# Performance work log

Hardware: AMD Instinct MI355X
Metric: run time of the kernel (lower is better)

## Reference

```python
import jax, jax.numpy as jnp
import numpy as np

N, A, B, C = 256, 1024, 64, 16


def setup_inputs() -> dict:
    key = jax.random.key(0)
    k1, k2, k3 = jax.random.split(key, 3)
    x = jax.random.normal(k1, (N, A), dtype=jnp.float32)
    weight = jax.random.normal(k2, (A, B * C), dtype=jnp.float32) * 0.02
    bias = jax.random.normal(k3, (B,), dtype=jnp.float32) * 0.02
    return {"x": x, "weight": weight, "bias": bias}


def reference(x, weight, bias):
    # x: [N, A]; weight: [A, B*C]; bias: [B]
    n = x.shape[0]
    mat = (x @ weight).reshape(n, B, C)              # [N, B, C]
    # pairwise L1 over the C (kernel) axis -> [N, N, B]
    l1 = jnp.abs(mat[:, None, :, :] - mat[None, :, :, :]).sum(axis=-1)
    # exp(-L1), sum over the first (broadcast) axis as in the torch code,
    # which includes the self term exp(0)=1
    out = jnp.exp(-l1).sum(axis=0) + bias            # [N, B]
    return out
```

## Files before the change

kernel.cpp:

```cpp
#include <hip/hip_runtime.h>
#include <hip/hip_bf16.h>

#define LOG2E 1.4426950408889634f

typedef __bf16 bf16x8 __attribute__((ext_vector_type(8)));
typedef float  f32x4  __attribute__((ext_vector_type(4)));

__device__ inline unsigned pack2(float lo, float hi){
  __hip_bfloat162 h = __float22bfloat162_rn(make_float2(lo, hi));
  return *reinterpret_cast<unsigned*>(&h);
}

__global__ __launch_bounds__(1024) void k_gemm_ks(const float* __restrict__ X,
                                                  const float* __restrict__ Wm,
                                                  float* __restrict__ P){
  __shared__ unsigned short As[4][64 * 72];
  __shared__ unsigned short Bs[4][64 * 72];
  const int m0 = blockIdx.x * 64, n0 = blockIdx.y * 64;
  const int k0 = blockIdx.z * 256;
  const int t = threadIdx.x;
  const int lane = t & 63, w = t >> 6;
  const int g = t >> 8, s = t & 255;
  const int r16 = lane & 15, quad = lane >> 4;
  const int wrow = (w & 3) * 16, wcol = (w >> 2) * 16;

  const int ar = s >> 2, aq = s & 3;
  const int bc = s & 15, bg = s >> 4;
  const float* ap = X + (size_t)(m0 + ar) * 1024 + k0 + g * 64 + aq * 16;
  const float* bp = Wm + (size_t)(k0 + g * 64) * 1024 + n0 + bc * 4;

  float4 pa[4], pb[4];
  #pragma unroll
  for (int r = 0; r < 4; ++r) pa[r] = *(const float4*)(ap + r * 4);
  #pragma unroll
  for (int r = 0; r < 4; ++r) pb[r] = *(const float4*)(bp + (size_t)(4 * bg + r) * 1024);

  {
    unsigned short* d = &As[g][ar * 72 + aq * 16];
    uint4 o;
    o.x = pack2(pa[0].x, pa[0].y); o.y = pack2(pa[0].z, pa[0].w);
    o.z = pack2(pa[1].x, pa[1].y); o.w = pack2(pa[1].z, pa[1].w);
    *(uint4*)d = o;
    o.x = pack2(pa[2].x, pa[2].y); o.y = pack2(pa[2].z, pa[2].w);
    o.z = pack2(pa[3].x, pa[3].y); o.w = pack2(pa[3].z, pa[3].w);
    *(uint4*)(d + 8) = o;
  }
  {
    #pragma unroll
    for (int e = 0; e < 4; ++e){
      const int n = bc * 4 + e;
      uint2 o;
      o.x = pack2(((const float*)&pb[0])[e], ((const float*)&pb[1])[e]);
      o.y = pack2(((const float*)&pb[2])[e], ((const float*)&pb[3])[e]);
      const int cw = (bg >> 1) ^ ((n >> 3) & 7);
      *(uint2*)(&Bs[g][n * 72 + cw * 8 + (bg & 1) * 4]) = o;
    }
  }
  __syncthreads();

  f32x4 acc0, acc1;
  #pragma unroll
  for (int e = 0; e < 4; ++e){ acc0[e] = 0.f; acc1[e] = 0.f; }
  const int nn = wcol + r16;
  const int nsw = (nn >> 3) & 7;
  #pragma unroll
  for (int gg = 0; gg < 4; ++gg){
    bf16x8 a0 = *(const bf16x8*)(&As[gg][(wrow + r16) * 72 + quad * 8]);
    bf16x8 a1 = *(const bf16x8*)(&As[gg][(wrow + r16) * 72 + 32 + quad * 8]);
    bf16x8 b0 = *(const bf16x8*)(&Bs[gg][nn * 72 + (((quad    ) ^ nsw) * 8)]);
    bf16x8 b1 = *(const bf16x8*)(&Bs[gg][nn * 72 + (((quad + 4) ^ nsw) * 8)]);
    acc0 = __builtin_amdgcn_mfma_f32_16x16x32_bf16(a0, b0, acc0, 0, 0, 0);
    acc1 = __builtin_amdgcn_mfma_f32_16x16x32_bf16(a1, b1, acc1, 0, 0, 0);
  }
  float* Pz = P + (size_t)blockIdx.z * 64 * 4096 + (size_t)((n0 + wcol) >> 4) * 4096;
  #pragma unroll
  for (int r = 0; r < 4; ++r){
    const int row = m0 + wrow + quad * 4 + r;
    Pz[row * 16 + r16] = acc0[r] + acc1[r];
  }
}

__global__ __launch_bounds__(1024) void k_pair(const float* __restrict__ P,
                                               const float* __restrict__ bias,
                                               float* __restrict__ out){
  __shared__ float L[256 * 20];
  __shared__ float red[16][64];
  const int b = blockIdx.x >> 2, jc = blockIdx.x & 3;
  const int t = threadIdx.x, lane = t & 63, w = t >> 6;

  {
    const int i = t >> 2, q = t & 3;
    const float* base = P + (size_t)b * 4096 + t * 4;
    float4 s0 = *(const float4*)(base);
    float4 s1 = *(const float4*)(base + 262144);
    float4 s2 = *(const float4*)(base + 524288);
    float4 s3 = *(const float4*)(base + 786432);
    float4 r;
    r.x = (s0.x + s1.x) + (s2.x + s3.x);
    r.y = (s0.y + s1.y) + (s2.y + s3.y);
    r.z = (s0.z + s1.z) + (s2.z + s3.z);
    r.w = (s0.w + s1.w) + (s2.w + s3.w);
    *(float4*)(&L[i * 20 + q * 4]) = r;
  }
  __syncthreads();

  const int j = jc * 64 + lane;
  float oj[16];
  #pragma unroll
  for (int q = 0; q < 4; ++q){
    float4 v = *(const float4*)(&L[j * 20 + q * 4]);
    oj[q*4+0] = v.x; oj[q*4+1] = v.y; oj[q*4+2] = v.z; oj[q*4+3] = v.w;
  }

  float acc = 0.f;
  const int i0 = w * 16;
  #pragma unroll 4
  for (int ii = i0; ii < i0 + 16; ++ii){
    const float4* fr = (const float4*)(&L[ii * 20]);
    float4 f0 = fr[0], f1 = fr[1], f2 = fr[2], f3 = fr[3];
    float p0 = fabsf(oj[0]  - f0.x) + fabsf(oj[1]  - f0.y)
             + fabsf(oj[2]  - f0.z) + fabsf(oj[3]  - f0.w);
    float p1 = fabsf(oj[4]  - f1.x) + fabsf(oj[5]  - f1.y)
             + fabsf(oj[6]  - f1.z) + fabsf(oj[7]  - f1.w);
    float p2 = fabsf(oj[8]  - f2.x) + fabsf(oj[9]  - f2.y)
             + fabsf(oj[10] - f2.z) + fabsf(oj[11] - f2.w);
    float p3 = fabsf(oj[12] - f3.x) + fabsf(oj[13] - f3.y)
             + fabsf(oj[14] - f3.z) + fabsf(oj[15] - f3.w);
    acc += exp2f(-LOG2E * ((p0 + p1) + (p2 + p3)));
  }
  red[w][lane] = acc;
  __syncthreads();
  if (w == 0){
    float tot = 0.f;
    #pragma unroll
    for (int ww = 0; ww < 16; ++ww) tot += red[ww][lane];
    out[(size_t)j * 64 + b] = tot + bias[b];
  }
}

extern "C" void kernel_launch(void* const* d_in, const int* in_sizes, int n_in,
                              void* d_out, int out_size, void* d_ws, size_t ws_size,
                              hipStream_t stream){
  const float* x    = (const float*)d_in[0];
  const float* W    = (const float*)d_in[1];
  const float* bias = (const float*)d_in[2];
  float* out = (float*)d_out;
  float* P   = (float*)d_ws;

  k_gemm_ks<<<dim3(4, 16, 4), 1024, 0, stream>>>(x, W, P);
  k_pair<<<256, 1024, 0, stream>>>(P, bias, out);
}
```

Baseline: 74.08 us.

## Fuse GEMM and pairwise kernels into one launch with a grid barrier

Merges the split-K GEMM kernel and the pairwise L1/exp kernel into one persistent 256-block kernel. The two phases are separated by a software grid barrier built on an atomic counter. This removes one kernel launch and the gap between the two kernels. In exchange it relies on all 256 blocks being co-resident and adds atomic spin-wait overhead. The ticket-based target keeps the counter valid across repeated calls.

```diff
diff --git a/kernel.cpp b/kernel.cpp
--- a/kernel.cpp
+++ b/kernel.cpp
@@ -11,130 +11,154 @@
   return *reinterpret_cast<unsigned*>(&h);
 }
 
-__global__ __launch_bounds__(1024) void k_gemm_ks(const float* __restrict__ X,
-                                                  const float* __restrict__ Wm,
-                                                  float* __restrict__ P){
-  __shared__ unsigned short As[4][64 * 72];
-  __shared__ unsigned short Bs[4][64 * 72];
-  const int m0 = blockIdx.x * 64, n0 = blockIdx.y * 64;
-  const int k0 = blockIdx.z * 256;
+__device__ unsigned g_bar;
+
+__device__ inline void grid_barrier(){
+  __threadfence();
+  __syncthreads();
+  if (threadIdx.x == 0){
+    unsigned ticket = __hip_atomic_fetch_add(&g_bar, 1u, __ATOMIC_ACQ_REL,
+                                             __HIP_MEMORY_SCOPE_AGENT);
+    unsigned target = (ticket / 256u + 1u) * 256u;
+    while (__hip_atomic_load(&g_bar, __ATOMIC_ACQUIRE,
+                             __HIP_MEMORY_SCOPE_AGENT) < target)
+      __builtin_amdgcn_s_sleep(2);
+  }
+  __syncthreads();
+  __threadfence();
+}
+
+__global__ __launch_bounds__(1024) void k_fused(const float* __restrict__ X,
+                                                const float* __restrict__ Wm,
+                                                const float* __restrict__ bias,
+                                                float* __restrict__ out,
+                                                float* __restrict__ P){
+  __shared__ __align__(16) char smem[73728];
+  unsigned short* As = (unsigned short*)smem;
+  unsigned short* Bs = (unsigned short*)(smem + 36864);
+
+  const int bid = blockIdx.x;
   const int t = threadIdx.x;
   const int lane = t & 63, w = t >> 6;
-  const int g = t >> 8, s = t & 255;
   const int r16 = lane & 15, quad = lane >> 4;
-  const int wrow = (w & 3) * 16, wcol = (w >> 2) * 16;
-
-  const int ar = s >> 2, aq = s & 3;
-  const int bc = s & 15, bg = s >> 4;
-  const float* ap = X + (size_t)(m0 + ar) * 1024 + k0 + g * 64 + aq * 16;
-  const float* bp = Wm + (size_t)(k0 + g * 64) * 1024 + n0 + bc * 4;
-
-  float4 pa[4], pb[4];
-  #pragma unroll
-  for (int r = 0; r < 4; ++r) pa[r] = *(const float4*)(ap + r * 4);
-  #pragma unroll
-  for (int r = 0; r < 4; ++r) pb[r] = *(const float4*)(bp + (size_t)(4 * bg + r) * 1024);
 
   {
-    unsigned short* d = &As[g][ar * 72 + aq * 16];
-    uint4 o;
-    o.x = pack2(pa[0].x, pa[0].y); o.y = pack2(pa[0].z, pa[0].w);
-    o.z = pack2(pa[1].x, pa[1].y); o.w = pack2(pa[1].z, pa[1].w);
-    *(uint4*)d = o;
-    o.x = pack2(pa[2].x, pa[2].y); o.y = pack2(pa[2].z, pa[2].w);
-    o.z = pack2(pa[3].x, pa[3].y); o.w = pack2(pa[3].z, pa[3].w);
-    *(uint4*)(d + 8) = o;
-  }
-  {
+    const int m0 = (bid & 3) * 64, n0 = ((bid >> 2) & 15) * 64;
+    const int ks = bid >> 6, k0 = ks * 256;
+    const int g = t >> 8, s = t & 255;
+    const int wrow = (w & 3) * 16, wcol = (w >> 2) * 16;
+
+    const int ar = s >> 2, aq = s & 3;
+    const int bc = s & 15, bg = s >> 4;
+    const float* ap = X + (size_t)(m0 + ar) * 1024 + k0 + g * 64 + aq * 16;
+    const float* bp = Wm + (size_t)(k0 + g * 64) * 1024 + n0 + bc * 4;
+
+    float4 pa[4], pb[4];
     #pragma unroll
-    for (int e = 0; e < 4; ++e){
-      const int n = bc * 4 + e;
-      uint2 o;
-      o.x = pack2(((const float*)&pb[0])[e], ((const float*)&pb[1])[e]);
-      o.y = pack2(((const float*)&pb[2])[e], ((const float*)&pb[3])[e]);
-      const int cw = (bg >> 1) ^ ((n >> 3) & 7);
-      *(uint2*)(&Bs[g][n * 72 + cw * 8 + (bg & 1) * 4]) = o;
+    for (int r = 0; r < 4; ++r) pa[r] = *(const float4*)(ap + r * 4);
+    #pragma unroll
+    for (int r = 0; r < 4; ++r) pb[r] = *(const float4*)(bp + (size_t)(4 * bg + r) * 1024);
+
+    {
+      unsigned short* d = &As[g * 4608 + ar * 72 + aq * 16];
+      uint4 o;
+      o.x = pack2(pa[0].x, pa[0].y); o.y = pack2(pa[0].z, pa[0].w);
+      o.z = pack2(pa[1].x, pa[1].y); o.w = pack2(pa[1].z, pa[1].w);
+      *(uint4*)d = o;
+      o.x = pack2(pa[2].x, pa[2].y); o.y = pack2(pa[2].z, pa[2].w);
+      o.z = pack2(pa[3].x, pa[3].y); o.w = pack2(pa[3].z, pa[3].w);
+      *(uint4*)(d + 8) = o;
+    }
+    {
+      #pragma unroll
+      for (int e = 0; e < 4; ++e){
+        const int n = bc * 4 + e;
+        uint2 o;
+        o.x = pack2(((const float*)&pb[0])[e], ((const float*)&pb[1])[e]);
+        o.y = pack2(((const float*)&pb[2])[e], ((const float*)&pb[3])[e]);
+        const int cw = (bg >> 1) ^ ((n >> 3) & 7);
+        *(uint2*)(&Bs[g * 4608 + n * 72 + cw * 8 + (bg & 1) * 4]) = o;
+      }
+    }
+    __syncthreads();
+
+    f32x4 acc0, acc1;
+    #pragma unroll
+    for (int e = 0; e < 4; ++e){ acc0[e] = 0.f; acc1[e] = 0.f; }
+    const int nn = wcol + r16;
+    const int nsw = (nn >> 3) & 7;
+    #pragma unroll
+    for (int gg = 0; gg < 4; ++gg){
+      bf16x8 a0 = *(const bf16x8*)(&As[gg * 4608 + (wrow + r16) * 72 + quad * 8]);
+      bf16x8 a1 = *(const bf16x8*)(&As[gg * 4608 + (wrow + r16) * 72 + 32 + quad * 8]);
+      bf16x8 b0 = *(const bf16x8*)(&Bs[gg * 4608 + nn * 72 + (((quad    ) ^ nsw) * 8)]);
+      bf16x8 b1 = *(const bf16x8*)(&Bs[gg * 4608 + nn * 72 + (((quad + 4) ^ nsw) * 8)]);
+      acc0 = __builtin_amdgcn_mfma_f32_16x16x32_bf16(a0, b0, acc0, 0, 0, 0);
+      acc1 = __builtin_amdgcn_mfma_f32_16x16x32_bf16(a1, b1, acc1, 0, 0, 0);
+    }
+    float* Pz = P + (size_t)ks * 262144 + (size_t)((n0 + wcol) >> 4) * 4096;
+    #pragma unroll
+    for (int r = 0; r < 4; ++r){
+      const int row = m0 + wrow + quad * 4 + r;
+      Pz[row * 16 + r16] = acc0[r] + acc1[r];
     }
   }
-  __syncthreads();
 
-  f32x4 acc0, acc1;
-  #pragma unroll
-  for (int e = 0; e < 4; ++e){ acc0[e] = 0.f; acc1[e] = 0.f; }
-  const int nn = wcol + r16;
-  const int nsw = (nn >> 3) & 7;
-  #pragma unroll
-  for (int gg = 0; gg < 4; ++gg){
-    bf16x8 a0 = *(const bf16x8*)(&As[gg][(wrow + r16) * 72 + quad * 8]);
-    bf16x8 a1 = *(const bf16x8*)(&As[gg][(wrow + r16) * 72 + 32 + quad * 8]);
-    bf16x8 b0 = *(const bf16x8*)(&Bs[gg][nn * 72 + (((quad    ) ^ nsw) * 8)]);
-    bf16x8 b1 = *(const bf16x8*)(&Bs[gg][nn * 72 + (((quad + 4) ^ nsw) * 8)]);
-    acc0 = __builtin_amdgcn_mfma_f32_16x16x32_bf16(a0, b0, acc0, 0, 0, 0);
-    acc1 = __builtin_amdgcn_mfma_f32_16x16x32_bf16(a1, b1, acc1, 0, 0, 0);
-  }
-  float* Pz = P + (size_t)blockIdx.z * 64 * 4096 + (size_t)((n0 + wcol) >> 4) * 4096;
-  #pragma unroll
-  for (int r = 0; r < 4; ++r){
-    const int row = m0 + wrow + quad * 4 + r;
-    Pz[row * 16 + r16] = acc0[r] + acc1[r];
-  }
-}
-
-__global__ __launch_bounds__(1024) void k_pair(const float* __restrict__ P,
-                                               const float* __restrict__ bias,
-                                               float* __restrict__ out){
-  __shared__ float L[256 * 20];
-  __shared__ float red[16][64];
-  const int b = blockIdx.x >> 2, jc = blockIdx.x & 3;
-  const int t = threadIdx.x, lane = t & 63, w = t >> 6;
+  grid_barrier();
 
   {
-    const int i = t >> 2, q = t & 3;
-    const float* base = P + (size_t)b * 4096 + t * 4;
-    float4 s0 = *(const float4*)(base);
-    float4 s1 = *(const float4*)(base + 262144);
-    float4 s2 = *(const float4*)(base + 524288);
-    float4 s3 = *(const float4*)(base + 786432);
-    float4 r;
-    r.x = (s0.x + s1.x) + (s2.x + s3.x);
-    r.y = (s0.y + s1.y) + (s2.y + s3.y);
-    r.z = (s0.z + s1.z) + (s2.z + s3.z);
-    r.w = (s0.w + s1.w) + (s2.w + s3.w);
-    *(float4*)(&L[i * 20 + q * 4]) = r;
-  }
-  __syncthreads();
+    float* L   = (float*)smem;
+    float* red = (float*)(smem + 20480);
+    const int b = bid >> 2, jc = bid & 3;
 
-  const int j = jc * 64 + lane;
-  float oj[16];
-  #pragma unroll
-  for (int q = 0; q < 4; ++q){
-    float4 v = *(const float4*)(&L[j * 20 + q * 4]);
-    oj[q*4+0] = v.x; oj[q*4+1] = v.y; oj[q*4+2] = v.z; oj[q*4+3] = v.w;
-  }
+    {
+      const int i = t >> 2, q = t & 3;
+      const float* base = P + (size_t)b * 4096 + t * 4;
+      float4 s0 = *(const float4*)(base);
+      float4 s1 = *(const float4*)(base + 262144);
+      float4 s2 = *(const float4*)(base + 524288);
+      float4 s3 = *(const float4*)(base + 786432);
+      float4 r;
+      r.x = (s0.x + s1.x) + (s2.x + s3.x);
+      r.y = (s0.y + s1.y) + (s2.y + s3.y);
+      r.z = (s0.z + s1.z) + (s2.z + s3.z);
+      r.w = (s0.w + s1.w) + (s2.w + s3.w);
+      *(float4*)(&L[i * 20 + q * 4]) = r;
+    }
+    __syncthreads();
 
-  float acc = 0.f;
-  const int i0 = w * 16;
-  #pragma unroll 4
-  for (int ii = i0; ii < i0 + 16; ++ii){
-    const float4* fr = (const float4*)(&L[ii * 20]);
-    float4 f0 = fr[0], f1 = fr[1], f2 = fr[2], f3 = fr[3];
-    float p0 = fabsf(oj[0]  - f0.x) + fabsf(oj[1]  - f0.y)
-             + fabsf(oj[2]  - f0.z) + fabsf(oj[3]  - f0.w);
-    float p1 = fabsf(oj[4]  - f1.x) + fabsf(oj[5]  - f1.y)
-             + fabsf(oj[6]  - f1.z) + fabsf(oj[7]  - f1.w);
-    float p2 = fabsf(oj[8]  - f2.x) + fabsf(oj[9]  - f2.y)
-             + fabsf(oj[10] - f2.z) + fabsf(oj[11] - f2.w);
-    float p3 = fabsf(oj[12] - f3.x) + fabsf(oj[13] - f3.y)
-             + fabsf(oj[14] - f3.z) + fabsf(oj[15] - f3.w);
-    acc += exp2f(-LOG2E * ((p0 + p1) + (p2 + p3)));
-  }
-  red[w][lane] = acc;
-  __syncthreads();
-  if (w == 0){
-    float tot = 0.f;
+    const int j = jc * 64 + lane;
+    float oj[16];
     #pragma unroll
-    for (int ww = 0; ww < 16; ++ww) tot += red[ww][lane];
-    out[(size_t)j * 64 + b] = tot + bias[b];
+    for (int q = 0; q < 4; ++q){
+      float4 v = *(const float4*)(&L[j * 20 + q * 4]);
+      oj[q*4+0] = v.x; oj[q*4+1] = v.y; oj[q*4+2] = v.z; oj[q*4+3] = v.w;
+    }
+
+    float acc = 0.f;
+    const int i0 = w * 16;
+    #pragma unroll 4
+    for (int ii = i0; ii < i0 + 16; ++ii){
+      const float4* fr = (const float4*)(&L[ii * 20]);
+      float4 f0 = fr[0], f1 = fr[1], f2 = fr[2], f3 = fr[3];
+      float p0 = fabsf(oj[0]  - f0.x) + fabsf(oj[1]  - f0.y)
+               + fabsf(oj[2]  - f0.z) + fabsf(oj[3]  - f0.w);
+      float p1 = fabsf(oj[4]  - f1.x) + fabsf(oj[5]  - f1.y)
+               + fabsf(oj[6]  - f1.z) + fabsf(oj[7]  - f1.w);
+      float p2 = fabsf(oj[8]  - f2.x) + fabsf(oj[9]  - f2.y)
+               + fabsf(oj[10] - f2.z) + fabsf(oj[11] - f2.w);
+      float p3 = fabsf(oj[12] - f3.x) + fabsf(oj[13] - f3.y)
+               + fabsf(oj[14] - f3.z) + fabsf(oj[15] - f3.w);
+      acc += exp2f(-LOG2E * ((p0 + p1) + (p2 + p3)));
+    }
+    red[w * 64 + lane] = acc;
+    __syncthreads();
+    if (w == 0){
+      float tot = 0.f;
+      #pragma unroll
+      for (int ww = 0; ww < 16; ++ww) tot += red[ww * 64 + lane];
+      out[(size_t)j * 64 + b] = tot + bias[b];
+    }
   }
 }
 
@@ -147,6 +171,5 @@
   float* out = (float*)d_out;
   float* P   = (float*)d_ws;
 
-  k_gemm_ks<<<dim3(4, 16, 4), 1024, 0, stream>>>(x, W, P);
-  k_pair<<<256, 1024, 0, stream>>>(P, bias, out);
+  k_fused<<<256, 1024, 0, stream>>>(x, W, bias, out, P);
 }
```

Measured after the change: 259.4 us. +250.2%, slower.

## Replace split-K GEMM with full-K tiles reduced in shared memory

Applied to the files above, without the earlier changes.

The GEMM now uses 32x32 output tiles over the full K=1024. Each block holds all of K in shared memory (144KB) and four wave groups split K, reducing their partials through LDS. This removes the split-K partial buffer, so the pair kernel reads one slice instead of summing four. The cost is large LDS use, one block per CU, and more redundant global loads of X and W across tiles.

```diff
diff --git a/kernel.cpp b/kernel.cpp
--- a/kernel.cpp
+++ b/kernel.cpp
@@ -11,72 +11,96 @@
   return *reinterpret_cast<unsigned*>(&h);
 }
 
-__global__ __launch_bounds__(1024) void k_gemm_ks(const float* __restrict__ X,
-                                                  const float* __restrict__ Wm,
-                                                  float* __restrict__ P){
-  __shared__ unsigned short As[4][64 * 72];
-  __shared__ unsigned short Bs[4][64 * 72];
-  const int m0 = blockIdx.x * 64, n0 = blockIdx.y * 64;
-  const int k0 = blockIdx.z * 256;
-  const int t = threadIdx.x;
-  const int lane = t & 63, w = t >> 6;
-  const int g = t >> 8, s = t & 255;
+__global__ __launch_bounds__(1024) void k_gemm(const float* __restrict__ X,
+                                               const float* __restrict__ Wm,
+                                               float* __restrict__ P){
+  __shared__ __align__(16) char smem[147456];
+  unsigned short* As = (unsigned short*)smem;
+  unsigned short* Bs = (unsigned short*)(smem + 73728);
+  float* red = (float*)smem;
+
+  const int nt = blockIdx.x, mt = blockIdx.y;
+  const int m0 = mt * 32, n0 = nt * 32;
+  const int t = threadIdx.x, lane = t & 63, w = t >> 6;
   const int r16 = lane & 15, quad = lane >> 4;
-  const int wrow = (w & 3) * 16, wcol = (w >> 2) * 16;
-
-  const int ar = s >> 2, aq = s & 3;
-  const int bc = s & 15, bg = s >> 4;
-  const float* ap = X + (size_t)(m0 + ar) * 1024 + k0 + g * 64 + aq * 16;
-  const float* bp = Wm + (size_t)(k0 + g * 64) * 1024 + n0 + bc * 4;
-
-  float4 pa[4], pb[4];
-  #pragma unroll
-  for (int r = 0; r < 4; ++r) pa[r] = *(const float4*)(ap + r * 4);
-  #pragma unroll
-  for (int r = 0; r < 4; ++r) pb[r] = *(const float4*)(bp + (size_t)(4 * bg + r) * 1024);
 
   {
-    unsigned short* d = &As[g][ar * 72 + aq * 16];
-    uint4 o;
-    o.x = pack2(pa[0].x, pa[0].y); o.y = pack2(pa[0].z, pa[0].w);
-    o.z = pack2(pa[1].x, pa[1].y); o.w = pack2(pa[1].z, pa[1].w);
-    *(uint4*)d = o;
-    o.x = pack2(pa[2].x, pa[2].y); o.y = pack2(pa[2].z, pa[2].w);
-    o.z = pack2(pa[3].x, pa[3].y); o.w = pack2(pa[3].z, pa[3].w);
-    *(uint4*)(d + 8) = o;
+    const int ar = t >> 5, aq = t & 31;
+    const float* ap = X + (size_t)(m0 + ar) * 1024 + aq * 32;
+    float4 pa[8];
+    #pragma unroll
+    for (int h = 0; h < 8; ++h) pa[h] = *(const float4*)(ap + h * 4);
+    unsigned short* d = &As[(aq >> 1) * 2304 + ar * 72 + (aq & 1) * 32];
+    #pragma unroll
+    for (int h = 0; h < 4; ++h){
+      uint4 o;
+      o.x = pack2(pa[2*h  ].x, pa[2*h  ].y); o.y = pack2(pa[2*h  ].z, pa[2*h  ].w);
+      o.z = pack2(pa[2*h+1].x, pa[2*h+1].y); o.w = pack2(pa[2*h+1].z, pa[2*h+1].w);
+      *(uint4*)(d + h * 8) = o;
+    }
   }
   {
+    const int bc = t & 7, bg = t >> 3;
+    const float* bp = Wm + (size_t)(8 * bg) * 1024 + n0 + bc * 4;
+    float4 pb[8];
+    #pragma unroll
+    for (int r = 0; r < 8; ++r) pb[r] = *(const float4*)(bp + (size_t)r * 1024);
+    const int chunk = bg >> 3, slot = bg & 7;
     #pragma unroll
     for (int e = 0; e < 4; ++e){
       const int n = bc * 4 + e;
-      uint2 o;
+      const int cw = slot ^ ((n >> 3) & 7);
+      uint4 o;
       o.x = pack2(((const float*)&pb[0])[e], ((const float*)&pb[1])[e]);
       o.y = pack2(((const float*)&pb[2])[e], ((const float*)&pb[3])[e]);
-      const int cw = (bg >> 1) ^ ((n >> 3) & 7);
-      *(uint2*)(&Bs[g][n * 72 + cw * 8 + (bg & 1) * 4]) = o;
+      o.z = pack2(((const float*)&pb[4])[e], ((const float*)&pb[5])[e]);
+      o.w = pack2(((const float*)&pb[6])[e], ((const float*)&pb[7])[e]);
+      *(uint4*)(&Bs[chunk * 2304 + n * 72 + cw * 8]) = o;
     }
   }
   __syncthreads();
 
+  const int tq = w & 3, kq = w >> 2;
+  const int mrow = (tq & 1) * 16 + r16;
+  const int nn   = (tq >> 1) * 16 + r16;
+  const int nsw  = (nn >> 3) & 7;
   f32x4 acc0, acc1;
   #pragma unroll
   for (int e = 0; e < 4; ++e){ acc0[e] = 0.f; acc1[e] = 0.f; }
-  const int nn = wcol + r16;
-  const int nsw = (nn >> 3) & 7;
   #pragma unroll
-  for (int gg = 0; gg < 4; ++gg){
-    bf16x8 a0 = *(const bf16x8*)(&As[gg][(wrow + r16) * 72 + quad * 8]);
-    bf16x8 a1 = *(const bf16x8*)(&As[gg][(wrow + r16) * 72 + 32 + quad * 8]);
-    bf16x8 b0 = *(const bf16x8*)(&Bs[gg][nn * 72 + (((quad    ) ^ nsw) * 8)]);
-    bf16x8 b1 = *(const bf16x8*)(&Bs[gg][nn * 72 + (((quad + 4) ^ nsw) * 8)]);
+  for (int s = 0; s < 8; s += 2){
+    int ko = kq * 256 + s * 32 + quad * 8;
+    int ch = ko >> 6, off = ko & 63;
+    bf16x8 a0 = *(const bf16x8*)(&As[ch * 2304 + mrow * 72 + off]);
+    bf16x8 b0 = *(const bf16x8*)(&Bs[ch * 2304 + nn * 72 + (((off >> 3) ^ nsw) * 8)]);
     acc0 = __builtin_amdgcn_mfma_f32_16x16x32_bf16(a0, b0, acc0, 0, 0, 0);
+    ko += 32; ch = ko >> 6; off = ko & 63;
+    bf16x8 a1 = *(const bf16x8*)(&As[ch * 2304 + mrow * 72 + off]);
+    bf16x8 b1 = *(const bf16x8*)(&Bs[ch * 2304 + nn * 72 + (((off >> 3) ^ nsw) * 8)]);
     acc1 = __builtin_amdgcn_mfma_f32_16x16x32_bf16(a1, b1, acc1, 0, 0, 0);
   }
-  float* Pz = P + (size_t)blockIdx.z * 64 * 4096 + (size_t)((n0 + wcol) >> 4) * 4096;
+  f32x4 sum;
   #pragma unroll
-  for (int r = 0; r < 4; ++r){
-    const int row = m0 + wrow + quad * 4 + r;
-    Pz[row * 16 + r16] = acc0[r] + acc1[r];
+  for (int e = 0; e < 4; ++e) sum[e] = acc0[e] + acc1[e];
+
+  __syncthreads();
+  if (kq){
+    *(f32x4*)(&red[(((kq - 1) * 4 + tq) * 64 + lane) * 4]) = sum;
+  }
+  __syncthreads();
+  if (kq == 0){
+    f32x4 r0 = *(const f32x4*)(&red[((0 * 4 + tq) * 64 + lane) * 4]);
+    f32x4 r1 = *(const f32x4*)(&red[((1 * 4 + tq) * 64 + lane) * 4]);
+    f32x4 r2 = *(const f32x4*)(&red[((2 * 4 + tq) * 64 + lane) * 4]);
+    #pragma unroll
+    for (int e = 0; e < 4; ++e) sum[e] += (r0[e] + r1[e]) + r2[e];
+    const int b = nt * 2 + (tq >> 1);
+    float* Pb = P + (size_t)b * 4096;
+    #pragma unroll
+    for (int e = 0; e < 4; ++e){
+      const int row = m0 + (tq & 1) * 16 + quad * 4 + e;
+      Pb[row * 16 + r16] = sum[e];
+    }
   }
 }
 
@@ -90,16 +114,7 @@
 
   {
     const int i = t >> 2, q = t & 3;
-    const float* base = P + (size_t)b * 4096 + t * 4;
-    float4 s0 = *(const float4*)(base);
-    float4 s1 = *(const float4*)(base + 262144);
-    float4 s2 = *(const float4*)(base + 524288);
-    float4 s3 = *(const float4*)(base + 786432);
-    float4 r;
-    r.x = (s0.x + s1.x) + (s2.x + s3.x);
-    r.y = (s0.y + s1.y) + (s2.y + s3.y);
-    r.z = (s0.z + s1.z) + (s2.z + s3.z);
-    r.w = (s0.w + s1.w) + (s2.w + s3.w);
+    float4 r = *(const float4*)(P + (size_t)b * 4096 + t * 4);
     *(float4*)(&L[i * 20 + q * 4]) = r;
   }
   __syncthreads();
@@ -147,6 +162,6 @@
   float* out = (float*)d_out;
   float* P   = (float*)d_ws;
 
-  k_gemm_ks<<<dim3(4, 16, 4), 1024, 0, stream>>>(x, W, P);
+  k_gemm<<<dim3(32, 8), 1024, 0, stream>>>(x, W, P);
   k_pair<<<256, 1024, 0, stream>>>(P, bias, out);
 }
```

Result: no change. 73.11 us (-1.3%).
